# Kernel tuning notes

Hardware: AMD Instinct MI355X
Metric: run time of the kernel (lower is better)

## Reference

```python
import jax, jax.numpy as jnp
import numpy as np
import math

B, H, W, CIN = 4, 64, 64, 256
G, C, K = 8, 32, 9
MAX_SCALE = 6.0


def setup_inputs() -> dict:
    key = jax.random.key(0)
    ks = jax.random.split(key, 10)
    s = 0.02
    x = jax.random.normal(ks[0], (B, H, W, CIN), dtype=jnp.float32)
    # linear params stored as [in, out]
    v_w = jax.random.normal(ks[1], (CIN, G * C), dtype=jnp.float32) * s
    v_b = jax.random.normal(ks[2], (G * C,), dtype=jnp.float32) * s
    qd_w = jax.random.normal(ks[3], (CIN, G * K * 2), dtype=jnp.float32) * s
    qd_b = jax.random.normal(ks[4], (G * K * 2,), dtype=jnp.float32) * s
    qs_w = jax.random.normal(ks[5], (CIN, G * K), dtype=jnp.float32) * s  # no bias
    qw_w = jax.random.normal(ks[6], (CIN, G * K), dtype=jnp.float32) * s
    qw_b = jax.random.normal(ks[7], (G * K,), dtype=jnp.float32) * s
    out_w = jax.random.normal(ks[8], (G * C, CIN), dtype=jnp.float32) * s
    out_b = jax.random.normal(ks[9], (CIN,), dtype=jnp.float32) * s
    # deformables_prior: 3x3 grid in [-1,1], meshgrid indexing='xy', stacked (x,y)
    n = int(math.isqrt(K))
    d = np.linspace(-1.0, 1.0, n, dtype=np.float32)
    gx, gy = np.meshgrid(d, d, indexing='xy')
    prior = jnp.asarray(np.stack([gx, gy], axis=-1).reshape(1, 1, 1, 1, K, 2))
    # deformables_scale: per-group inverse-sigmoid of (i+1)/G - 1e-4
    sc = np.array([(i + 1) / G - 1e-4 for i in range(G)], dtype=np.float32)
    dscale = jnp.asarray(np.log(sc / (1.0 - sc)).reshape(1, 1, 1, G, 1, 1))
    return dict(x=x, v_w=v_w, v_b=v_b, qd_w=qd_w, qd_b=qd_b, qs_w=qs_w,
                qw_w=qw_w, qw_b=qw_b, out_w=out_w, out_b=out_b,
                prior=prior, dscale=dscale)


def _dcn_sample(v, deform, weights):
    # v: [B,H,W,G,C]; deform: [B,H,W,G,K,2] pixel offsets (x,y); weights: [B,H,W,G,K]
    b_, h_, w_, g_, c_ = v.shape
    ww = jnp.arange(w_, dtype=v.dtype)[None, None, :, None, None]
    hh = jnp.arange(h_, dtype=v.dtype)[None, :, None, None, None]
    px = ww + deform[..., 0]  # [B,H,W,G,K]
    py = hh + deform[..., 1]
    x0 = jnp.floor(px); y0 = jnp.floor(py)
    wx1 = px - x0; wx0 = 1.0 - wx1
    wy1 = py - y0; wy0 = 1.0 - wy1
    bidx = jnp.arange(b_)[:, None, None, None, None]
    gidx = jnp.arange(g_)[None, None, None, :, None]

    def gather(yi, xi):
        valid = ((yi >= 0) & (yi < h_) & (xi >= 0) & (xi < w_)).astype(v.dtype)
        yc = jnp.clip(yi, 0, h_ - 1).astype(jnp.int32)
        xc = jnp.clip(xi, 0, w_ - 1).astype(jnp.int32)
        return v[bidx, yc, xc, gidx] * valid[..., None]  # [B,H,W,G,K,C]

    samp = (gather(y0, x0) * (wy0 * wx0)[..., None]
            + gather(y0, x0 + 1) * (wy0 * wx1)[..., None]
            + gather(y0 + 1, x0) * (wy1 * wx0)[..., None]
            + gather(y0 + 1, x0 + 1) * (wy1 * wx1)[..., None])
    # weighted sum over kernels -> [B,H,W,G,C]
    return jnp.einsum('bhwgkc,bhwgk->bhwgc', samp, weights)


def reference(x, v_w, v_b, qd_w, qd_b, qs_w, qw_w, qw_b, out_w, out_b, prior, dscale):
    b_, h_, w_, _ = x.shape
    v = (x @ v_w + v_b).reshape(b_, h_, w_, G, C)
    deform = (x @ qd_w + qd_b).reshape(b_, h_, w_, G, K, 2)
    scale = (x @ qs_w).reshape(b_, h_, w_, G, K, 1) + dscale
    deform = (deform + prior) * jax.nn.sigmoid(scale) * MAX_SCALE
    weights = (x @ qw_w + qw_b).reshape(b_, h_, w_, G, K)
    out = _dcn_sample(v, deform, weights)  # [B,H,W,G,C]
    out = out.reshape(b_, h_, w_, G * C)
    return out @ out_w + out_b
```

## Files before the change

kernel.cpp:

```cpp
#include <hip/hip_runtime.h>

#define NPIX 16384

typedef __attribute__((ext_vector_type(8))) short short8;
typedef __attribute__((ext_vector_type(4))) float f32x4;

__device__ __forceinline__ unsigned short f2bf(float f) {
    unsigned u = __float_as_uint(f);
    unsigned r = (u + 0x7fffu + ((u >> 16) & 1u)) >> 16;
    return (unsigned short)r;
}

#define GLOAD16(SRC, DST) \
    __builtin_amdgcn_global_load_lds( \
        (const __attribute__((address_space(1))) unsigned*)(SRC), \
        (__attribute__((address_space(3))) unsigned*)(DST), 16, 0, 0)

__global__ __launch_bounds__(256) void prep_x(const float* __restrict__ x,
                                              unsigned short* __restrict__ xb)
{
    const size_t i = (size_t)blockIdx.x * 256 + threadIdx.x;
    const float4 v0 = *(const float4*)(x + i * 8);
    const float4 v1 = *(const float4*)(x + i * 8 + 4);
    unsigned r0 = f2bf(v0.x) | ((unsigned)f2bf(v0.y) << 16);
    unsigned r1 = f2bf(v0.z) | ((unsigned)f2bf(v0.w) << 16);
    unsigned r2 = f2bf(v1.x) | ((unsigned)f2bf(v1.y) << 16);
    unsigned r3 = f2bf(v1.z) | ((unsigned)f2bf(v1.w) << 16);
    *(uint4*)(xb + i * 8) = make_uint4(r0, r1, r2, r3);
}

__global__ __launch_bounds__(256) void prep_w(
    const float* __restrict__ v_w, const float* __restrict__ qd_w,
    const float* __restrict__ qs_w, const float* __restrict__ qw_w,
    const float* __restrict__ out_w, const float* __restrict__ qd_b,
    const float* __restrict__ qw_b,
    unsigned short* __restrict__ WtV, unsigned short* __restrict__ WtD,
    unsigned short* __restrict__ WtO, float* __restrict__ biasD)
{
    const int n = blockIdx.x;
    const int k = threadIdx.x;
    if (n < 256) {
        WtV[n * 256 + k] = f2bf(v_w[k * 256 + n]);
    } else if (n < 576) {
        const int nd = n - 256;
        float val = 0.f;
        if (nd < 144)      val = qd_w[k * 144 + nd];
        else if (nd < 216) val = qs_w[k * 72 + (nd - 144)];
        else if (nd < 288) val = qw_w[k * 72 + (nd - 216)];
        WtD[nd * 256 + k] = f2bf(val);
    } else if (n < 832) {
        const int no = n - 576;
        WtO[no * 256 + k] = f2bf(out_w[k * 256 + no]);
    } else {
        for (int i = k; i < 320; i += 256) {
            float bv = 0.f;
            if (i < 144)                 bv = qd_b[i];
            else if (i >= 216 && i < 288) bv = qw_b[i - 216];
            biasD[i] = bv;
        }
    }
}

template<int NCT, bool BF16OUT>
__global__ __launch_bounds__(256) void gemm_mfma(
    const unsigned short* __restrict__ A,
    const unsigned short* __restrict__ Wt,
    const float* __restrict__ bias,
    void* __restrict__ Yv)
{
    constexpr int NCOL = NCT * 64;
    __shared__ unsigned short As[64 * 256];
    __shared__ unsigned short Bs[64 * 256];

    const int tid  = threadIdx.x;
    const int wid  = tid >> 6;
    const int lane = tid & 63;
    const int row0 = blockIdx.x * 64;
    const int col0 = blockIdx.y * 64;

    const unsigned short* Ab = A  + (size_t)row0 * 256;
    const unsigned short* Bb = Wt + (size_t)col0 * 256;
    const int rl = lane >> 5;
    const int gl = lane & 31;

    #pragma unroll
    for (int it = 0; it < 8; ++it) {
        const int r   = wid * 16 + it * 2 + rl;
        const int gsw = gl ^ (r & 7);
        GLOAD16(Ab + r * 256 + gsw * 8, &As[(wid * 16 + it * 2) * 256]);
        GLOAD16(Bb + r * 256 + gsw * 8, &Bs[(wid * 16 + it * 2) * 256]);
    }
    asm volatile("s_waitcnt vmcnt(0)" ::: "memory");
    __syncthreads();

    f32x4 acc00 = {0,0,0,0}, acc01 = {0,0,0,0};
    f32x4 acc10 = {0,0,0,0}, acc11 = {0,0,0,0};

    const int wr = (wid >> 1) * 32;
    const int wc = (wid & 1) * 32;
    const int fr = lane & 15;
    const int fg = lane >> 4;

    const int ra0 = wr + fr, ra1 = ra0 + 16;
    const int rb0 = wc + fr, rb1 = rb0 + 16;
    const int sa  = ra0 & 7;
    const int sb  = rb0 & 7;

    #pragma unroll
    for (int t = 0; t < 8; ++t) {
        const int gran = t * 4 + fg;
        short8 a0 = *(const short8*)&As[ra0 * 256 + (gran ^ sa) * 8];
        short8 a1 = *(const short8*)&As[ra1 * 256 + (gran ^ sa) * 8];
        short8 b0 = *(const short8*)&Bs[rb0 * 256 + (gran ^ sb) * 8];
        short8 b1 = *(const short8*)&Bs[rb1 * 256 + (gran ^ sb) * 8];
        acc00 = __builtin_amdgcn_mfma_f32_16x16x32_bf16(a0, b0, acc00, 0, 0, 0);
        acc01 = __builtin_amdgcn_mfma_f32_16x16x32_bf16(a0, b1, acc01, 0, 0, 0);
        acc10 = __builtin_amdgcn_mfma_f32_16x16x32_bf16(a1, b0, acc10, 0, 0, 0);
        acc11 = __builtin_amdgcn_mfma_f32_16x16x32_bf16(a1, b1, acc11, 0, 0, 0);
    }

    const int colA = col0 + wc + fr;
    const int colB = colA + 16;
    const float biasA = bias[colA];
    const float biasB = bias[colB];

    #pragma unroll
    for (int jj = 0; jj < 4; ++jj) {
        const int r0a = row0 + wr + fg * 4 + jj;
        const int r1a = r0a + 16;
        float v00 = acc00[jj] + biasA;
        float v01 = acc01[jj] + biasB;
        float v10 = acc10[jj] + biasA;
        float v11 = acc11[jj] + biasB;
        if (BF16OUT) {
            unsigned short* Y = (unsigned short*)Yv;
            Y[(size_t)r0a * NCOL + colA] = f2bf(v00);
            Y[(size_t)r0a * NCOL + colB] = f2bf(v01);
            Y[(size_t)r1a * NCOL + colA] = f2bf(v10);
            Y[(size_t)r1a * NCOL + colB] = f2bf(v11);
        } else {
            float* Y = (float*)Yv;
            Y[(size_t)r0a * NCOL + colA] = v00;
            Y[(size_t)r0a * NCOL + colB] = v01;
            Y[(size_t)r1a * NCOL + colA] = v10;
            Y[(size_t)r1a * NCOL + colB] = v11;
        }
    }
}

__global__ __launch_bounds__(256) void dcn_sample2(
    const unsigned short* __restrict__ vbuf,
    const float* __restrict__ proj,
    const float* __restrict__ prior,
    const float* __restrict__ dscale,
    unsigned short* __restrict__ mid)
{
    __shared__ int   offs[288 * 4];
    __shared__ float wts [288 * 4];

    const int tid  = threadIdx.x;
    const int pix0 = blockIdx.x * 4;

    for (int it = tid; it < 288; it += 256) {
        const int p   = it / 72;
        const int rem = it - p * 72;
        const int g   = rem / 9;
        const int k   = rem - g * 9;
        const int pix = pix0 + p;
        const int b   = pix >> 12;
        const int hw  = pix & 4095;
        const int h   = hw >> 6, w = hw & 63;

        const float* row = proj + (size_t)pix * 320;
        const float qdx = row[g * 18 + k * 2 + 0];
        const float qdy = row[g * 18 + k * 2 + 1];
        const float s   = row[144 + g * 9 + k] + dscale[g];
        const float wt  = row[216 + g * 9 + k];
        const float sig6 = 6.0f / (1.0f + __expf(-s));
        const float px = (float)w + (qdx + prior[k * 2 + 0]) * sig6;
        const float py = (float)h + (qdy + prior[k * 2 + 1]) * sig6;

        const float x0f = floorf(px), y0f = floorf(py);
        const int ix = (int)x0f, iy = (int)y0f;
        const float wx1 = px - x0f, wx0 = 1.f - wx1;
        const float wy1 = py - y0f, wy0 = 1.f - wy1;
        const int base_b = b << 12;

        #pragma unroll
        for (int tp = 0; tp < 4; ++tp) {
            const int yy = iy + (tp >> 1), xx = ix + (tp & 1);
            const bool valid = (yy >= 0) & (yy < 64) & (xx >= 0) & (xx < 64);
            const int yc = min(max(yy, 0), 63), xc = min(max(xx, 0), 63);
            const float wgt = wt * ((tp >> 1) ? wy1 : wy0) * ((tp & 1) ? wx1 : wx0);
            offs[it * 4 + tp] = ((base_b + yc * 64 + xc) << 8) + g * 32;
            wts [it * 4 + tp] = valid ? wgt : 0.f;
        }
    }
    __syncthreads();

    const int p = tid >> 6;
    const int g = (tid >> 3) & 7;
    const int q = tid & 7;
    const int c0 = q * 4;
    const int item0 = p * 72 + g * 9;

    float a0 = 0.f, a1 = 0.f, a2 = 0.f, a3 = 0.f;
    #pragma unroll
    for (int k = 0; k < 9; ++k) {
        const int it4 = (item0 + k) * 4;
        const int4   o4 = *(const int4*)&offs[it4];
        const float4 w4 = *(const float4*)&wts[it4];
        {
            const uint2 r = *(const uint2*)(vbuf + o4.x + c0);
            a0 = fmaf(w4.x, __uint_as_float(r.x << 16), a0);
            a1 = fmaf(w4.x, __uint_as_float(r.x & 0xffff0000u), a1);
            a2 = fmaf(w4.x, __uint_as_float(r.y << 16), a2);
            a3 = fmaf(w4.x, __uint_as_float(r.y & 0xffff0000u), a3);
        }
        {
            const uint2 r = *(const uint2*)(vbuf + o4.y + c0);
            a0 = fmaf(w4.y, __uint_as_float(r.x << 16), a0);
            a1 = fmaf(w4.y, __uint_as_float(r.x & 0xffff0000u), a1);
            a2 = fmaf(w4.y, __uint_as_float(r.y << 16), a2);
            a3 = fmaf(w4.y, __uint_as_float(r.y & 0xffff0000u), a3);
        }
        {
            const uint2 r = *(const uint2*)(vbuf + o4.z + c0);
            a0 = fmaf(w4.z, __uint_as_float(r.x << 16), a0);
            a1 = fmaf(w4.z, __uint_as_float(r.x & 0xffff0000u), a1);
            a2 = fmaf(w4.z, __uint_as_float(r.y << 16), a2);
            a3 = fmaf(w4.z, __uint_as_float(r.y & 0xffff0000u), a3);
        }
        {
            const uint2 r = *(const uint2*)(vbuf + o4.w + c0);
            a0 = fmaf(w4.w, __uint_as_float(r.x << 16), a0);
            a1 = fmaf(w4.w, __uint_as_float(r.x & 0xffff0000u), a1);
            a2 = fmaf(w4.w, __uint_as_float(r.y << 16), a2);
            a3 = fmaf(w4.w, __uint_as_float(r.y & 0xffff0000u), a3);
        }
    }

    const int pix = pix0 + p;
    unsigned short* mp = mid + (size_t)pix * 256 + g * 32 + c0;
    const unsigned lo = f2bf(a0) | ((unsigned)f2bf(a1) << 16);
    const unsigned hi = f2bf(a2) | ((unsigned)f2bf(a3) << 16);
    *(uint2*)mp = make_uint2(lo, hi);
}

extern "C" void kernel_launch(void* const* d_in, const int* in_sizes, int n_in,
                              void* d_out, int out_size, void* d_ws, size_t ws_size,
                              hipStream_t stream)
{
    (void)in_sizes; (void)n_in; (void)out_size; (void)ws_size;

    const float* x      = (const float*)d_in[0];
    const float* v_w    = (const float*)d_in[1];
    const float* v_b    = (const float*)d_in[2];
    const float* qd_w   = (const float*)d_in[3];
    const float* qd_b   = (const float*)d_in[4];
    const float* qs_w   = (const float*)d_in[5];
    const float* qw_w   = (const float*)d_in[6];
    const float* qw_b   = (const float*)d_in[7];
    const float* out_w  = (const float*)d_in[8];
    const float* out_b  = (const float*)d_in[9];
    const float* prior  = (const float*)d_in[10];
    const float* dscale = (const float*)d_in[11];
    float* out = (float*)d_out;

    char* ws = (char*)d_ws;
    unsigned short* xb    = (unsigned short*)(ws);
    unsigned short* v_bf  = (unsigned short*)(ws + 8388608);
    float*          proj  = (float*)(ws + 16777216);
    unsigned short* mid   = (unsigned short*)(ws + 37748736);
    unsigned short* WtV   = (unsigned short*)(ws + 46137344);
    unsigned short* WtD   = (unsigned short*)(ws + 46268416);
    unsigned short* WtO   = (unsigned short*)(ws + 46432256);
    float*          biasD = (float*)(ws + 46563328);

    prep_x<<<dim3(2048), dim3(256), 0, stream>>>(x, xb);
    prep_w<<<dim3(833), dim3(256), 0, stream>>>(v_w, qd_w, qs_w, qw_w, out_w,
                                                qd_b, qw_b, WtV, WtD, WtO, biasD);

    gemm_mfma<4, true ><<<dim3(256, 4), dim3(256), 0, stream>>>(xb, WtV, v_b, v_bf);
    gemm_mfma<5, false><<<dim3(256, 5), dim3(256), 0, stream>>>(xb, WtD, biasD, proj);

    dcn_sample2<<<dim3(NPIX / 4), dim3(256), 0, stream>>>(v_bf, proj, prior, dscale, mid);

    gemm_mfma<4, false><<<dim3(256, 4), dim3(256), 0, stream>>>(mid, WtO, out_b, out);
}
```

Measured before the change: 61.25 us.

## Fuse x conversion into merged projection GEMM, tile weight transpose, widen sampling

Drops the separate x-to-bf16 kernel: the merged projection GEMM now reads fp32 x directly and converts it while filling LDS. It also merges the value and deform/scale/weight projections into one 9-column-tile launch. Weight preparation becomes a single tiled-transpose kernel through shared memory with coalesced accesses, producing one concatenated weight buffer. The sampling kernel handles 8 pixels per block, stages the projection rows in LDS, and uses 16-byte gathers of 8 channels per thread. The cost is that each of the 9 column tiles re-reads and re-converts fp32 x, doubling A-side traffic per tile, in exchange for fewer launches and no xb intermediate.

```diff
diff --git a/kernel.cpp b/kernel.cpp
--- a/kernel.cpp
+++ b/kernel.cpp
@@ -16,59 +16,66 @@
         (const __attribute__((address_space(1))) unsigned*)(SRC), \
         (__attribute__((address_space(3))) unsigned*)(DST), 16, 0, 0)
 
-__global__ __launch_bounds__(256) void prep_x(const float* __restrict__ x,
-                                              unsigned short* __restrict__ xb)
-{
-    const size_t i = (size_t)blockIdx.x * 256 + threadIdx.x;
-    const float4 v0 = *(const float4*)(x + i * 8);
-    const float4 v1 = *(const float4*)(x + i * 8 + 4);
-    unsigned r0 = f2bf(v0.x) | ((unsigned)f2bf(v0.y) << 16);
-    unsigned r1 = f2bf(v0.z) | ((unsigned)f2bf(v0.w) << 16);
-    unsigned r2 = f2bf(v1.x) | ((unsigned)f2bf(v1.y) << 16);
-    unsigned r3 = f2bf(v1.z) | ((unsigned)f2bf(v1.w) << 16);
-    *(uint4*)(xb + i * 8) = make_uint4(r0, r1, r2, r3);
-}
-
-__global__ __launch_bounds__(256) void prep_w(
+__device__ __forceinline__ float wsrc(int k, int n,
+    const float* v_w, const float* qd_w, const float* qs_w,
+    const float* qw_w, const float* out_w)
+{
+    if (n < 256) return v_w[k * 256 + n];
+    n -= 256;
+    if (n < 144) return qd_w[k * 144 + n];
+    n -= 144;
+    if (n < 72)  return qs_w[k * 72 + n];
+    n -= 72;
+    if (n < 72)  return qw_w[k * 72 + n];
+    n -= 72;
+    if (n < 32)  return 0.f;
+    return out_w[k * 256 + (n - 32)];
+}
+
+__global__ __launch_bounds__(256) void prep_wt(
     const float* __restrict__ v_w, const float* __restrict__ qd_w,
     const float* __restrict__ qs_w, const float* __restrict__ qw_w,
     const float* __restrict__ out_w, const float* __restrict__ qd_b,
     const float* __restrict__ qw_b,
-    unsigned short* __restrict__ WtV, unsigned short* __restrict__ WtD,
-    unsigned short* __restrict__ WtO, float* __restrict__ biasD)
-{
-    const int n = blockIdx.x;
-    const int k = threadIdx.x;
-    if (n < 256) {
-        WtV[n * 256 + k] = f2bf(v_w[k * 256 + n]);
-    } else if (n < 576) {
-        const int nd = n - 256;
-        float val = 0.f;
-        if (nd < 144)      val = qd_w[k * 144 + nd];
-        else if (nd < 216) val = qs_w[k * 72 + (nd - 144)];
-        else if (nd < 288) val = qw_w[k * 72 + (nd - 216)];
-        WtD[nd * 256 + k] = f2bf(val);
-    } else if (n < 832) {
-        const int no = n - 576;
-        WtO[no * 256 + k] = f2bf(out_w[k * 256 + no]);
-    } else {
-        for (int i = k; i < 320; i += 256) {
+    unsigned short* __restrict__ Wt, float* __restrict__ biasD)
+{
+    const int tid = threadIdx.x;
+    if (blockIdx.x == 52) {
+        for (int i = tid; i < 320; i += 256) {
             float bv = 0.f;
-            if (i < 144)                 bv = qd_b[i];
+            if (i < 144)                  bv = qd_b[i];
             else if (i >= 216 && i < 288) bv = qw_b[i - 216];
             biasD[i] = bv;
         }
-    }
-}
-
-template<int NCT, bool BF16OUT>
-__global__ __launch_bounds__(256) void gemm_mfma(
-    const unsigned short* __restrict__ A,
-    const unsigned short* __restrict__ Wt,
-    const float* __restrict__ bias,
-    void* __restrict__ Yv)
-{
-    constexpr int NCOL = NCT * 64;
+        return;
+    }
+    __shared__ float t[64][65];
+    const int tn = blockIdx.x % 13;
+    const int tk = blockIdx.x / 13;
+    #pragma unroll
+    for (int i = 0; i < 16; ++i) {
+        const int idx = tid + i * 256;
+        const int r = idx >> 6;
+        const int c = idx & 63;
+        t[r][c] = wsrc(tk * 64 + r, tn * 64 + c, v_w, qd_w, qs_w, qw_w, out_w);
+    }
+    __syncthreads();
+    #pragma unroll
+    for (int i = 0; i < 8; ++i) {
+        const int idx = tid + i * 256;
+        const int rn = idx >> 5;
+        const int cc = idx & 31;
+        const unsigned pk = (unsigned)f2bf(t[cc * 2][rn])
+                          | ((unsigned)f2bf(t[cc * 2 + 1][rn]) << 16);
+        ((unsigned*)(Wt + (size_t)(tn * 64 + rn) * 256 + tk * 64))[cc] = pk;
+    }
+}
+
+__global__ __launch_bounds__(256) void gemm_proj(
+    const float* __restrict__ x, const unsigned short* __restrict__ Wt,
+    const float* __restrict__ v_b, const float* __restrict__ biasD,
+    unsigned short* __restrict__ v_bf, float* __restrict__ proj)
+{
     __shared__ unsigned short As[64 * 256];
     __shared__ unsigned short Bs[64 * 256];
 
@@ -76,19 +83,32 @@
     const int wid  = tid >> 6;
     const int lane = tid & 63;
     const int row0 = blockIdx.x * 64;
-    const int col0 = blockIdx.y * 64;
-
-    const unsigned short* Ab = A  + (size_t)row0 * 256;
-    const unsigned short* Bb = Wt + (size_t)col0 * 256;
+    const int j    = blockIdx.y;
+
+    const unsigned short* Bb = Wt + (size_t)(j * 64) * 256;
     const int rl = lane >> 5;
     const int gl = lane & 31;
-
     #pragma unroll
     for (int it = 0; it < 8; ++it) {
-        const int r   = wid * 16 + it * 2 + rl;
-        const int gsw = gl ^ (r & 7);
-        GLOAD16(Ab + r * 256 + gsw * 8, &As[(wid * 16 + it * 2) * 256]);
-        GLOAD16(Bb + r * 256 + gsw * 8, &Bs[(wid * 16 + it * 2) * 256]);
+        const int rr  = wid * 16 + it * 2 + rl;
+        const int gsw = gl ^ (rr & 7);
+        GLOAD16(Bb + rr * 256 + gsw * 8, &Bs[(wid * 16 + it * 2) * 256]);
+    }
+
+    const float* Ab = x + (size_t)row0 * 256;
+    #pragma unroll
+    for (int it = 0; it < 8; ++it) {
+        const int idx = tid + it * 256;
+        const int r   = idx >> 5;
+        const int gg  = idx & 31;
+        const float4 u0 = *(const float4*)(Ab + r * 256 + gg * 8);
+        const float4 u1 = *(const float4*)(Ab + r * 256 + gg * 8 + 4);
+        uint4 pk;
+        pk.x = f2bf(u0.x) | ((unsigned)f2bf(u0.y) << 16);
+        pk.y = f2bf(u0.z) | ((unsigned)f2bf(u0.w) << 16);
+        pk.z = f2bf(u1.x) | ((unsigned)f2bf(u1.y) << 16);
+        pk.w = f2bf(u1.z) | ((unsigned)f2bf(u1.w) << 16);
+        *(uint4*)&As[r * 256 + (gg ^ (r & 7)) * 8] = pk;
     }
     asm volatile("s_waitcnt vmcnt(0)" ::: "memory");
     __syncthreads();
@@ -119,49 +139,128 @@
         acc11 = __builtin_amdgcn_mfma_f32_16x16x32_bf16(a1, b1, acc11, 0, 0, 0);
     }
 
+    if (j < 4) {
+        const int colA = j * 64 + wc + fr;
+        const int colB = colA + 16;
+        const float biasA = v_b[colA];
+        const float biasB = v_b[colB];
+        #pragma unroll
+        for (int jj = 0; jj < 4; ++jj) {
+            const int r0a = row0 + wr + fg * 4 + jj;
+            const int r1a = r0a + 16;
+            v_bf[(size_t)r0a * 256 + colA] = f2bf(acc00[jj] + biasA);
+            v_bf[(size_t)r0a * 256 + colB] = f2bf(acc01[jj] + biasB);
+            v_bf[(size_t)r1a * 256 + colA] = f2bf(acc10[jj] + biasA);
+            v_bf[(size_t)r1a * 256 + colB] = f2bf(acc11[jj] + biasB);
+        }
+    } else {
+        const int colA = (j - 4) * 64 + wc + fr;
+        const int colB = colA + 16;
+        const float biasA = biasD[colA];
+        const float biasB = biasD[colB];
+        #pragma unroll
+        for (int jj = 0; jj < 4; ++jj) {
+            const int r0a = row0 + wr + fg * 4 + jj;
+            const int r1a = r0a + 16;
+            proj[(size_t)r0a * 320 + colA] = acc00[jj] + biasA;
+            proj[(size_t)r0a * 320 + colB] = acc01[jj] + biasB;
+            proj[(size_t)r1a * 320 + colA] = acc10[jj] + biasA;
+            proj[(size_t)r1a * 320 + colB] = acc11[jj] + biasB;
+        }
+    }
+}
+
+__global__ __launch_bounds__(256) void gemm_out(
+    const unsigned short* __restrict__ A, const unsigned short* __restrict__ WtO,
+    const float* __restrict__ bias, float* __restrict__ Y)
+{
+    __shared__ unsigned short As[64 * 256];
+    __shared__ unsigned short Bs[64 * 256];
+
+    const int tid  = threadIdx.x;
+    const int wid  = tid >> 6;
+    const int lane = tid & 63;
+    const int row0 = blockIdx.x * 64;
+    const int col0 = blockIdx.y * 64;
+
+    const unsigned short* Ab = A   + (size_t)row0 * 256;
+    const unsigned short* Bb = WtO + (size_t)col0 * 256;
+    const int rl = lane >> 5;
+    const int gl = lane & 31;
+
+    #pragma unroll
+    for (int it = 0; it < 8; ++it) {
+        const int r   = wid * 16 + it * 2 + rl;
+        const int gsw = gl ^ (r & 7);
+        GLOAD16(Ab + r * 256 + gsw * 8, &As[(wid * 16 + it * 2) * 256]);
+        GLOAD16(Bb + r * 256 + gsw * 8, &Bs[(wid * 16 + it * 2) * 256]);
+    }
+    asm volatile("s_waitcnt vmcnt(0)" ::: "memory");
+    __syncthreads();
+
+    f32x4 acc00 = {0,0,0,0}, acc01 = {0,0,0,0};
+    f32x4 acc10 = {0,0,0,0}, acc11 = {0,0,0,0};
+
+    const int wr = (wid >> 1) * 32;
+    const int wc = (wid & 1) * 32;
+    const int fr = lane & 15;
+    const int fg = lane >> 4;
+
+    const int ra0 = wr + fr, ra1 = ra0 + 16;
+    const int rb0 = wc + fr, rb1 = rb0 + 16;
+    const int sa  = ra0 & 7;
+    const int sb  = rb0 & 7;
+
+    #pragma unroll
+    for (int t = 0; t < 8; ++t) {
+        const int gran = t * 4 + fg;
+        short8 a0 = *(const short8*)&As[ra0 * 256 + (gran ^ sa) * 8];
+        short8 a1 = *(const short8*)&As[ra1 * 256 + (gran ^ sa) * 8];
+        short8 b0 = *(const short8*)&Bs[rb0 * 256 + (gran ^ sb) * 8];
+        short8 b1 = *(const short8*)&Bs[rb1 * 256 + (gran ^ sb) * 8];
+        acc00 = __builtin_amdgcn_mfma_f32_16x16x32_bf16(a0, b0, acc00, 0, 0, 0);
+        acc01 = __builtin_amdgcn_mfma_f32_16x16x32_bf16(a0, b1, acc01, 0, 0, 0);
+        acc10 = __builtin_amdgcn_mfma_f32_16x16x32_bf16(a1, b0, acc10, 0, 0, 0);
+        acc11 = __builtin_amdgcn_mfma_f32_16x16x32_bf16(a1, b1, acc11, 0, 0, 0);
+    }
+
     const int colA = col0 + wc + fr;
     const int colB = colA + 16;
     const float biasA = bias[colA];
     const float biasB = bias[colB];
-
     #pragma unroll
     for (int jj = 0; jj < 4; ++jj) {
         const int r0a = row0 + wr + fg * 4 + jj;
         const int r1a = r0a + 16;
-        float v00 = acc00[jj] + biasA;
-        float v01 = acc01[jj] + biasB;
-        float v10 = acc10[jj] + biasA;
-        float v11 = acc11[jj] + biasB;
-        if (BF16OUT) {
-            unsigned short* Y = (unsigned short*)Yv;
-            Y[(size_t)r0a * NCOL + colA] = f2bf(v00);
-            Y[(size_t)r0a * NCOL + colB] = f2bf(v01);
-            Y[(size_t)r1a * NCOL + colA] = f2bf(v10);
-            Y[(size_t)r1a * NCOL + colB] = f2bf(v11);
-        } else {
-            float* Y = (float*)Yv;
-            Y[(size_t)r0a * NCOL + colA] = v00;
-            Y[(size_t)r0a * NCOL + colB] = v01;
-            Y[(size_t)r1a * NCOL + colA] = v10;
-            Y[(size_t)r1a * NCOL + colB] = v11;
-        }
-    }
-}
-
-__global__ __launch_bounds__(256) void dcn_sample2(
+        Y[(size_t)r0a * 256 + colA] = acc00[jj] + biasA;
+        Y[(size_t)r0a * 256 + colB] = acc01[jj] + biasB;
+        Y[(size_t)r1a * 256 + colA] = acc10[jj] + biasA;
+        Y[(size_t)r1a * 256 + colB] = acc11[jj] + biasB;
+    }
+}
+
+__global__ __launch_bounds__(256) void dcn_sample3(
     const unsigned short* __restrict__ vbuf,
     const float* __restrict__ proj,
     const float* __restrict__ prior,
     const float* __restrict__ dscale,
     unsigned short* __restrict__ mid)
 {
-    __shared__ int   offs[288 * 4];
-    __shared__ float wts [288 * 4];
+    __shared__ float projs[8 * 320];
+    __shared__ int   offs[576 * 4];
+    __shared__ float wts [576 * 4];
 
     const int tid  = threadIdx.x;
-    const int pix0 = blockIdx.x * 4;
-
-    for (int it = tid; it < 288; it += 256) {
+    const int pix0 = blockIdx.x * 8;
+
+    for (int i = tid; i < 640; i += 256) {
+        const int p = i / 80, c = i - p * 80;
+        *(float4*)&projs[p * 320 + c * 4] =
+            *(const float4*)&proj[(size_t)(pix0 + p) * 320 + c * 4];
+    }
+    __syncthreads();
+
+    for (int it = tid; it < 576; it += 256) {
         const int p   = it / 72;
         const int rem = it - p * 72;
         const int g   = rem / 9;
@@ -171,7 +270,7 @@
         const int hw  = pix & 4095;
         const int h   = hw >> 6, w = hw & 63;
 
-        const float* row = proj + (size_t)pix * 320;
+        const float* row = &projs[p * 320];
         const float qdx = row[g * 18 + k * 2 + 0];
         const float qdy = row[g * 18 + k * 2 + 1];
         const float s   = row[144 + g * 9 + k] + dscale[g];
@@ -198,53 +297,42 @@
     }
     __syncthreads();
 
-    const int p = tid >> 6;
-    const int g = (tid >> 3) & 7;
-    const int q = tid & 7;
-    const int c0 = q * 4;
+    const int p  = tid >> 5;
+    const int g  = (tid >> 2) & 7;
+    const int q  = tid & 3;
+    const int c0 = q * 8;
     const int item0 = p * 72 + g * 9;
 
-    float a0 = 0.f, a1 = 0.f, a2 = 0.f, a3 = 0.f;
+    float a0=0.f,a1=0.f,a2=0.f,a3=0.f,a4=0.f,a5=0.f,a6=0.f,a7=0.f;
     #pragma unroll
     for (int k = 0; k < 9; ++k) {
         const int it4 = (item0 + k) * 4;
         const int4   o4 = *(const int4*)&offs[it4];
         const float4 w4 = *(const float4*)&wts[it4];
-        {
-            const uint2 r = *(const uint2*)(vbuf + o4.x + c0);
-            a0 = fmaf(w4.x, __uint_as_float(r.x << 16), a0);
-            a1 = fmaf(w4.x, __uint_as_float(r.x & 0xffff0000u), a1);
-            a2 = fmaf(w4.x, __uint_as_float(r.y << 16), a2);
-            a3 = fmaf(w4.x, __uint_as_float(r.y & 0xffff0000u), a3);
-        }
-        {
-            const uint2 r = *(const uint2*)(vbuf + o4.y + c0);
-            a0 = fmaf(w4.y, __uint_as_float(r.x << 16), a0);
-            a1 = fmaf(w4.y, __uint_as_float(r.x & 0xffff0000u), a1);
-            a2 = fmaf(w4.y, __uint_as_float(r.y << 16), a2);
-            a3 = fmaf(w4.y, __uint_as_float(r.y & 0xffff0000u), a3);
-        }
-        {
-            const uint2 r = *(const uint2*)(vbuf + o4.z + c0);
-            a0 = fmaf(w4.z, __uint_as_float(r.x << 16), a0);
-            a1 = fmaf(w4.z, __uint_as_float(r.x & 0xffff0000u), a1);
-            a2 = fmaf(w4.z, __uint_as_float(r.y << 16), a2);
-            a3 = fmaf(w4.z, __uint_as_float(r.y & 0xffff0000u), a3);
-        }
-        {
-            const uint2 r = *(const uint2*)(vbuf + o4.w + c0);
-            a0 = fmaf(w4.w, __uint_as_float(r.x << 16), a0);
-            a1 = fmaf(w4.w, __uint_as_float(r.x & 0xffff0000u), a1);
-            a2 = fmaf(w4.w, __uint_as_float(r.y << 16), a2);
-            a3 = fmaf(w4.w, __uint_as_float(r.y & 0xffff0000u), a3);
+        #pragma unroll
+        for (int tp = 0; tp < 4; ++tp) {
+            const int   off = (tp == 0) ? o4.x : (tp == 1) ? o4.y : (tp == 2) ? o4.z : o4.w;
+            const float wgt = (tp == 0) ? w4.x : (tp == 1) ? w4.y : (tp == 2) ? w4.z : w4.w;
+            const uint4 r = *(const uint4*)(vbuf + off + c0);
+            a0 = fmaf(wgt, __uint_as_float(r.x << 16),          a0);
+            a1 = fmaf(wgt, __uint_as_float(r.x & 0xffff0000u), a1);
+            a2 = fmaf(wgt, __uint_as_float(r.y << 16),          a2);
+            a3 = fmaf(wgt, __uint_as_float(r.y & 0xffff0000u), a3);
+            a4 = fmaf(wgt, __uint_as_float(r.z << 16),          a4);
+            a5 = fmaf(wgt, __uint_as_float(r.z & 0xffff0000u), a5);
+            a6 = fmaf(wgt, __uint_as_float(r.w << 16),          a6);
+            a7 = fmaf(wgt, __uint_as_float(r.w & 0xffff0000u), a7);
         }
     }
 
     const int pix = pix0 + p;
     unsigned short* mp = mid + (size_t)pix * 256 + g * 32 + c0;
-    const unsigned lo = f2bf(a0) | ((unsigned)f2bf(a1) << 16);
-    const unsigned hi = f2bf(a2) | ((unsigned)f2bf(a3) << 16);
-    *(uint2*)mp = make_uint2(lo, hi);
+    uint4 o;
+    o.x = f2bf(a0) | ((unsigned)f2bf(a1) << 16);
+    o.y = f2bf(a2) | ((unsigned)f2bf(a3) << 16);
+    o.z = f2bf(a4) | ((unsigned)f2bf(a5) << 16);
+    o.w = f2bf(a6) | ((unsigned)f2bf(a7) << 16);
+    *(uint4*)mp = o;
 }
 
 extern "C" void kernel_launch(void* const* d_in, const int* in_sizes, int n_in,
@@ -268,23 +356,18 @@
     float* out = (float*)d_out;
 
     char* ws = (char*)d_ws;
-    unsigned short* xb    = (unsigned short*)(ws);
-    unsigned short* v_bf  = (unsigned short*)(ws + 8388608);
-    float*          proj  = (float*)(ws + 16777216);
-    unsigned short* mid   = (unsigned short*)(ws + 37748736);
-    unsigned short* WtV   = (unsigned short*)(ws + 46137344);
-    unsigned short* WtD   = (unsigned short*)(ws + 46268416);
-    unsigned short* WtO   = (unsigned short*)(ws + 46432256);
-    float*          biasD = (float*)(ws + 46563328);
-
-    prep_x<<<dim3(2048), dim3(256), 0, stream>>>(x, xb);
-    prep_w<<<dim3(833), dim3(256), 0, stream>>>(v_w, qd_w, qs_w, qw_w, out_w,
-                                                qd_b, qw_b, WtV, WtD, WtO, biasD);
-
-    gemm_mfma<4, true ><<<dim3(256, 4), dim3(256), 0, stream>>>(xb, WtV, v_b, v_bf);
-    gemm_mfma<5, false><<<dim3(256, 5), dim3(256), 0, stream>>>(xb, WtD, biasD, proj);
-
-    dcn_sample2<<<dim3(NPIX / 4), dim3(256), 0, stream>>>(v_bf, proj, prior, dscale, mid);
-
-    gemm_mfma<4, false><<<dim3(256, 4), dim3(256), 0, stream>>>(mid, WtO, out_b, out);
-}
+    unsigned short* v_bf  = (unsigned short*)(ws);
+    float*          proj  = (float*)(ws + 8388608);
+    unsigned short* mid   = (unsigned short*)(ws + 29360128);
+    unsigned short* Wt    = (unsigned short*)(ws + 37748736);
+    float*          biasD = (float*)(ws + 38175744);
+
+    prep_wt<<<dim3(53), dim3(256), 0, stream>>>(v_w, qd_w, qs_w, qw_w, out_w,
+                                                qd_b, qw_b, Wt, biasD);
+
+    gemm_proj<<<dim3(256, 9), dim3(256), 0, stream>>>(x, Wt, v_b, biasD, v_bf, proj);
+
+    dcn_sample3<<<dim3(NPIX / 8), dim3(256), 0, stream>>>(v_bf, proj, prior, dscale, mid);
+
+    gemm_out<<<dim3(256, 4), dim3(256), 0, stream>>>(mid, Wt + 576 * 256, out_b, out);
+}
```

After: 65.65 us. 1.07x slower.
